# Kernel tuning notes

Measured on AMD Instinct MI355X. Metric: run time of the kernel, lower is better.

Reference implementation:

```python
import jax, jax.numpy as jnp
import numpy as np

R = 1  # local_window_radius (kernel = 2R+1 = 3)


def setup_inputs() -> dict:
    key = jax.random.key(0)
    ks = jax.random.split(key, 4)
    b, c, h, w, v = 4, 128, 96, 192, 2
    scale = 1.0 / np.sqrt(c).astype(np.float32)
    return {
        "feature0": jax.random.normal(ks[0], (b, c, h, w), jnp.float32),
        "flow": jax.random.normal(ks[1], (b, v, h, w), jnp.float32),
        "Wq": jax.random.normal(ks[2], (c, c), jnp.float32) * scale,
        "bq": jnp.zeros((c,), jnp.float32),
        "Wk": jax.random.normal(ks[3], (c, c), jnp.float32) * scale,
        "bk": jnp.zeros((c,), jnp.float32),
    }


def _windows(x, r):
    # x: [b, C, h, w] -> [b, h, w, C, k^2], zero-padded 3x3 neighborhoods.
    # Window element order matches F.unfold: row-major over (dy, dx).
    b, C, h, w = x.shape
    xp = jnp.pad(x, ((0, 0), (0, 0), (r, r), (r, r)))
    k = 2 * r + 1
    wins = [xp[:, :, dy:dy + h, dx:dx + w] for dy in range(k) for dx in range(k)]
    return jnp.stack(wins, axis=-1).transpose(0, 2, 3, 1, 4)


def reference(feature0, flow, Wq, bq, Wk, bk):
    b, c, h, w = feature0.shape
    f = feature0.transpose(0, 2, 3, 1)              # [b,h,w,c]
    q = f @ Wq.T + bq                                # q_proj -> [b,h,w,c]
    kproj = (f @ Wk.T + bk).transpose(0, 3, 1, 2)    # k_proj -> [b,c,h,w]
    k_win = _windows(kproj, R)                       # [b,h,w,c,k2]
    v_win = _windows(flow, R)                        # [b,h,w,v,k2]
    scores = jnp.einsum('bhwc,bhwck->bhwk', q, k_win) / jnp.sqrt(jnp.asarray(c, q.dtype))
    prob = jax.nn.softmax(scores, axis=-1)           # [b,h,w,k2]
    out = jnp.einsum('bhwk,bhwvk->bhwv', prob, v_win)
    return out.transpose(0, 3, 1, 2)                 # [b,v,h,w]
```

## Files before the change

kernel.cpp:

```cpp
#include <hip/hip_runtime.h>
#include <math.h>

#define B_   4
#define C_   128
#define H_   96
#define W_   192
#define HW_  (H_*W_)

#define TH 8
#define TW 16
#define HX 18
#define HPX 180
#define SHS 136

typedef __attribute__((ext_vector_type(8))) short bf16x8;
typedef __attribute__((ext_vector_type(4))) float f32x4;

__device__ __forceinline__ unsigned short f2bf(float f) {
    unsigned u = __float_as_uint(f);
    u = (u + 0x7FFFu + ((u >> 16) & 1u)) >> 16;
    return (unsigned short)u;
}
__device__ __forceinline__ float bflo(unsigned u) { return __uint_as_float(u << 16); }
__device__ __forceinline__ float bfhi(unsigned u) { return __uint_as_float(u & 0xFFFF0000u); }

__global__ __launch_bounds__(256) void prep_kernel(
    const float* __restrict__ Wq, const float* __restrict__ Wk,
    const float* __restrict__ bq, const float* __restrict__ bk,
    short* __restrict__ Apack, float* __restrict__ u2,
    float* __restrict__ v2, float* __restrict__ c0)
{
    if (blockIdx.x < 8) {
        const int rb   = blockIdx.x;
        const int t    = threadIdx.x;
        const int lane = t & 63;
        const int row  = rb * 16 + (lane & 15);
        const int colb = (t >> 6) * 32 + (lane >> 4) * 8;
        float a[8];
#pragma unroll
        for (int j = 0; j < 8; ++j) a[j] = 0.f;
        for (int c = 0; c < C_; ++c) {
            const float wk = Wk[c * C_ + row];
            const float4 w0 = *(const float4*)(Wq + c * C_ + colb);
            const float4 w1 = *(const float4*)(Wq + c * C_ + colb + 4);
            a[0] = fmaf(wk, w0.x, a[0]); a[1] = fmaf(wk, w0.y, a[1]);
            a[2] = fmaf(wk, w0.z, a[2]); a[3] = fmaf(wk, w0.w, a[3]);
            a[4] = fmaf(wk, w1.x, a[4]); a[5] = fmaf(wk, w1.y, a[5]);
            a[6] = fmaf(wk, w1.z, a[6]); a[7] = fmaf(wk, w1.w, a[7]);
        }
        bf16x8 v;
#pragma unroll
        for (int j = 0; j < 8; ++j) v[j] = (short)f2bf(a[j]);
        *(bf16x8*)(Apack + ((size_t)rb * 256 + t) * 8) = v;
    } else {
        const int t = threadIdx.x;
        if (t < 128) {
            float a = 0.f;
            for (int c = 0; c < C_; ++c) a = fmaf(Wk[c * C_ + t], bq[c], a);
            u2[t] = a;
        } else {
            const int i = t - 128;
            float a = 0.f;
            for (int c = 0; c < C_; ++c) a = fmaf(Wq[c * C_ + i], bk[c], a);
            v2[i] = a;
        }
        if (t == 0) {
            float a = 0.f;
            for (int c = 0; c < C_; ++c) a = fmaf(bq[c], bk[c], a);
            c0[0] = a;
        }
    }
}

__global__ __launch_bounds__(256, 3) void fused_kernel(
    const float* __restrict__ f, const short* __restrict__ Apack,
    const float* __restrict__ u2v, const float* __restrict__ v2v,
    const float* __restrict__ c0p, const float* __restrict__ flow,
    float* __restrict__ out)
{
    __shared__ unsigned short sH[HPX * SHS];
    __shared__ float sS[TH][TW][9];

    const int t    = threadIdx.x;
    const int lane = t & 63;
    const int w    = t >> 6;
    const int g    = lane >> 4, p = lane & 15;

    const int wg  = blockIdx.x;
    const int idx = (wg & 7) * 72 + (wg >> 3);
    const int b   = idx / 144;
    const int rem = idx - b * 144;
    const int ty  = rem / 12, tx = rem - ty * 12;
    const int y0  = ty * TH, x0 = tx * TW;
    const float* fb = f + (size_t)b * C_ * HW_;

#pragma unroll
    for (int it = 0; it < 12; ++it) {
        const int gi = it * 256 + t;
        if (gi < HPX * 16) {
            const int c8 = gi / HPX;
            const int px = gi - c8 * HPX;
            const int hy = px / HX;
            const int hx = px - hy * HX;
            const int gy = y0 + hy - 1, gx = x0 + hx - 1;
            bf16x8 v = {0, 0, 0, 0, 0, 0, 0, 0};
            if ((gy >= 0) && (gy < H_) && (gx >= 0) && (gx < W_)) {
                const float* src = fb + gy * W_ + gx;
#pragma unroll
                for (int j = 0; j < 8; ++j)
                    v[j] = (short)f2bf(src[(size_t)(c8 * 8 + j) * HW_]);
            }
            *(bf16x8*)(sH + px * SHS + c8 * 8) = v;
        }
    }
    __syncthreads();

    f32x4 acc[8][2];
#pragma unroll
    for (int rb = 0; rb < 8; ++rb)
#pragma unroll
        for (int cf = 0; cf < 2; ++cf) acc[rb][cf] = (f32x4){0.f, 0.f, 0.f, 0.f};

#pragma unroll
    for (int ks = 0; ks < 4; ++ks) {
        bf16x8 afr[8];
#pragma unroll
        for (int rb = 0; rb < 8; ++rb)
            afr[rb] = *(const bf16x8*)(Apack + ((size_t)((rb * 4 + ks) * 64 + lane)) * 8);
        bf16x8 bfr[2];
#pragma unroll
        for (int cf = 0; cf < 2; ++cf) {
            const int hpx = (2 * w + cf + 1) * HX + (p + 1);
            bfr[cf] = *(const bf16x8*)(sH + hpx * SHS + (ks * 4 + g) * 8);
        }
#pragma unroll
        for (int rb = 0; rb < 8; ++rb)
#pragma unroll
            for (int cf = 0; cf < 2; ++cf)
                acc[rb][cf] = __builtin_amdgcn_mfma_f32_16x16x32_bf16(
                    afr[rb], bfr[cf], acc[rb][cf], 0, 0, 0);
    }

    const int L0 = ((lane & 16) << 1) | p;
    const int L1 = L0 + 16;
    bf16x8 aS[2][4];
#pragma unroll
    for (int cf = 0; cf < 2; ++cf) {
        uint2 pk[8];
#pragma unroll
        for (int rb = 0; rb < 8; ++rb) {
            const f32x4 uu = *(const f32x4*)(u2v + rb * 16 + g * 4);
            const f32x4 vv = acc[rb][cf] + uu;
            pk[rb].x = (unsigned)f2bf(vv[0]) | ((unsigned)f2bf(vv[1]) << 16);
            pk[rb].y = (unsigned)f2bf(vv[2]) | ((unsigned)f2bf(vv[3]) << 16);
        }
#pragma unroll
        for (int ks = 0; ks < 4; ++ks) {
            int dw[4];
#pragma unroll
            for (int dd = 0; dd < 4; ++dd) {
                const int v0 = (dd & 1) ? (int)pk[2 * ks].y     : (int)pk[2 * ks].x;
                const int v1 = (dd & 1) ? (int)pk[2 * ks + 1].y : (int)pk[2 * ks + 1].x;
                const int sl = (dd & 2) ? L1 : L0;
                const int w0 = __shfl(v0, sl, 64);
                const int w1 = __shfl(v1, sl, 64);
                dw[dd] = (g & 2) ? w1 : w0;
            }
            int4 qv = make_int4(dw[0], dw[1], dw[2], dw[3]);
            aS[cf][ks] = *(bf16x8*)&qv;
        }
    }

#pragma unroll
    for (int cf = 0; cf < 2; ++cf) {
        const int y = 2 * w + cf;
#pragma unroll
        for (int dy = 0; dy < 3; ++dy) {
            const int hyy = y + dy;
            f32x4 s0 = (f32x4){0.f, 0.f, 0.f, 0.f};
            f32x4 s1 = (f32x4){0.f, 0.f, 0.f, 0.f};
#pragma unroll
            for (int ks = 0; ks < 4; ++ks) {
                const int hpx0 = hyy * HX + p;
                const bf16x8 b0 = *(const bf16x8*)(sH + hpx0 * SHS + (ks * 4 + g) * 8);
                const bf16x8 b1 = *(const bf16x8*)(sH + (hpx0 + 2) * SHS + (ks * 4 + g) * 8);
                s0 = __builtin_amdgcn_mfma_f32_16x16x32_bf16(aS[cf][ks], b0, s0, 0, 0, 0);
                s1 = __builtin_amdgcn_mfma_f32_16x16x32_bf16(aS[cf][ks], b1, s1, 0, 0, 0);
            }
#pragma unroll
            for (int i = 0; i < 4; ++i) {
                const int x = g * 4 + i;
                const float val = (g < 2) ? s0[i] : s1[i];
                const int   d   = (g < 2) ? (p - x) : (x - p);
                const int   n9  = (g < 2) ? (dy * 3 + d) : (dy * 3 + 2 - d);
                if ((unsigned)d <= 2u) sS[y][x][n9] = val;
            }
        }
    }

    const int r  = (lane >> 4) & 1;
    const int v  = lane >> 5;
    const int xl = lane & 15;
    const int yl = 2 * w + r;
    const int gy = y0 + yl, gx = x0 + xl;

    float beta = 0.f;
    const bool edge = (gx == 0) | (gx == W_ - 1) | (gy == 0) | (gy == H_ - 1);
    if (edge) {
        const int hpx = (yl + 1) * HX + (xl + 1);
#pragma unroll
        for (int c8 = 0; c8 < 16; ++c8) {
            const uint4 hv = *(const uint4*)(sH + hpx * SHS + c8 * 8);
            const float4 va = *(const float4*)(v2v + c8 * 8);
            const float4 vb = *(const float4*)(v2v + c8 * 8 + 4);
            beta += bflo(hv.x) * va.x + bfhi(hv.x) * va.y
                  + bflo(hv.y) * va.z + bfhi(hv.y) * va.w
                  + bflo(hv.z) * vb.x + bfhi(hv.z) * vb.y
                  + bflo(hv.w) * vb.z + bfhi(hv.w) * vb.w;
        }
        beta += *c0p;
    }

    const float scale = 0.08838834764831845f;
    float sv[9], mk[9];
    int spn[9];
    float m = -1e30f;
#pragma unroll
    for (int n = 0; n < 9; ++n) {
        const int yn = gy + n / 3 - 1, xn = gx + n % 3 - 1;
        const bool ok = (yn >= 0) && (yn < H_) && (xn >= 0) && (xn < W_);
        mk[n]  = ok ? 1.f : 0.f;
        spn[n] = ok ? yn * W_ + xn : gy * W_ + gx;
        sv[n]  = ok ? (sS[yl][xl][n] + beta) * scale : 0.f;
        m = fmaxf(m, sv[n]);
    }
    float e[9], sum = 0.f;
#pragma unroll
    for (int n = 0; n < 9; ++n) { e[n] = __expf(sv[n] - m); sum += e[n]; }
    const float inv = 1.f / sum;

    const float* f0 = flow + ((size_t)b * 2 + v) * HW_;
    float o = 0.f;
#pragma unroll
    for (int n = 0; n < 9; ++n) o += e[n] * mk[n] * f0[spn[n]];
    out[((size_t)b * 2 + v) * HW_ + gy * W_ + gx] = o * inv;
}

extern "C" void kernel_launch(void* const* d_in, const int* in_sizes, int n_in,
                              void* d_out, int out_size, void* d_ws, size_t ws_size,
                              hipStream_t stream) {
    const float* f   = (const float*)d_in[0];
    const float* flw = (const float*)d_in[1];
    const float* Wq  = (const float*)d_in[2];
    const float* bq  = (const float*)d_in[3];
    const float* Wk  = (const float*)d_in[4];
    const float* bk  = (const float*)d_in[5];
    float* out = (float*)d_out;

    short* Apack = (short*)d_ws;
    float* u2    = (float*)(Apack + 128 * 128);
    float* v2    = u2 + 128;
    float* c0    = v2 + 128;

    prep_kernel<<<9, 256, 0, stream>>>(Wq, Wk, bq, bk, Apack, u2, v2, c0);
    fused_kernel<<<576, 256, 0, stream>>>(f, Apack, u2, v2, c0, flw, out);
}
```

Measured before the change: 36.84 us.

## Use 512-thread blocks with one tile row per wave in fused kernel

Doubles the fused kernel's block size to 8 waves, with each wave handling one tile row instead of two. This halves per-wave MFMA accumulators and register pressure, and the halo load now spans all 512 threads. The prep kernel's weight-product loop is unrolled by four to batch its loads, and f32-to-bf16 conversion now uses the library intrinsic. In exchange, half the lanes in the final softmax and flow gather idle, and the larger blocks with high LDS use may limit how many blocks fit per CU.

```diff
diff --git a/kernel.cpp b/kernel.cpp
--- a/kernel.cpp
+++ b/kernel.cpp
@@ -1,4 +1,5 @@
 #include <hip/hip_runtime.h>
+#include <hip/hip_bf16.h>
 #include <math.h>
 
 #define B_   4
@@ -17,9 +18,8 @@
 typedef __attribute__((ext_vector_type(4))) float f32x4;
 
 __device__ __forceinline__ unsigned short f2bf(float f) {
-    unsigned u = __float_as_uint(f);
-    u = (u + 0x7FFFu + ((u >> 16) & 1u)) >> 16;
-    return (unsigned short)u;
+    __hip_bfloat16 h = __float2bfloat16(f);
+    return *(unsigned short*)&h;
 }
 __device__ __forceinline__ float bflo(unsigned u) { return __uint_as_float(u << 16); }
 __device__ __forceinline__ float bfhi(unsigned u) { return __uint_as_float(u & 0xFFFF0000u); }
@@ -39,14 +39,23 @@
         float a[8];
 #pragma unroll
         for (int j = 0; j < 8; ++j) a[j] = 0.f;
-        for (int c = 0; c < C_; ++c) {
-            const float wk = Wk[c * C_ + row];
-            const float4 w0 = *(const float4*)(Wq + c * C_ + colb);
-            const float4 w1 = *(const float4*)(Wq + c * C_ + colb + 4);
-            a[0] = fmaf(wk, w0.x, a[0]); a[1] = fmaf(wk, w0.y, a[1]);
-            a[2] = fmaf(wk, w0.z, a[2]); a[3] = fmaf(wk, w0.w, a[3]);
-            a[4] = fmaf(wk, w1.x, a[4]); a[5] = fmaf(wk, w1.y, a[5]);
-            a[6] = fmaf(wk, w1.z, a[6]); a[7] = fmaf(wk, w1.w, a[7]);
+#pragma unroll 2
+        for (int c = 0; c < C_; c += 4) {
+            float wk[4];
+            float4 wv[4][2];
+#pragma unroll
+            for (int u = 0; u < 4; ++u) {
+                wk[u] = Wk[(c + u) * C_ + row];
+                wv[u][0] = *(const float4*)(Wq + (c + u) * C_ + colb);
+                wv[u][1] = *(const float4*)(Wq + (c + u) * C_ + colb + 4);
+            }
+#pragma unroll
+            for (int u = 0; u < 4; ++u) {
+                a[0] = fmaf(wk[u], wv[u][0].x, a[0]); a[1] = fmaf(wk[u], wv[u][0].y, a[1]);
+                a[2] = fmaf(wk[u], wv[u][0].z, a[2]); a[3] = fmaf(wk[u], wv[u][0].w, a[3]);
+                a[4] = fmaf(wk[u], wv[u][1].x, a[4]); a[5] = fmaf(wk[u], wv[u][1].y, a[5]);
+                a[6] = fmaf(wk[u], wv[u][1].z, a[6]); a[7] = fmaf(wk[u], wv[u][1].w, a[7]);
+            }
         }
         bf16x8 v;
 #pragma unroll
@@ -72,7 +81,7 @@
     }
 }
 
-__global__ __launch_bounds__(256, 3) void fused_kernel(
+__global__ __launch_bounds__(512, 6) void fused_kernel(
     const float* __restrict__ f, const short* __restrict__ Apack,
     const float* __restrict__ u2v, const float* __restrict__ v2v,
     const float* __restrict__ c0p, const float* __restrict__ flow,
@@ -95,8 +104,8 @@
     const float* fb = f + (size_t)b * C_ * HW_;
 
 #pragma unroll
-    for (int it = 0; it < 12; ++it) {
-        const int gi = it * 256 + t;
+    for (int it = 0; it < 6; ++it) {
+        const int gi = it * 512 + t;
         if (gi < HPX * 16) {
             const int c8 = gi / HPX;
             const int px = gi - c8 * HPX;
@@ -115,99 +124,81 @@
     }
     __syncthreads();
 
-    f32x4 acc[8][2];
-#pragma unroll
-    for (int rb = 0; rb < 8; ++rb)
-#pragma unroll
-        for (int cf = 0; cf < 2; ++cf) acc[rb][cf] = (f32x4){0.f, 0.f, 0.f, 0.f};
+    f32x4 acc[8];
+#pragma unroll
+    for (int rb = 0; rb < 8; ++rb) acc[rb] = (f32x4){0.f, 0.f, 0.f, 0.f};
 
 #pragma unroll
     for (int ks = 0; ks < 4; ++ks) {
-        bf16x8 afr[8];
-#pragma unroll
-        for (int rb = 0; rb < 8; ++rb)
-            afr[rb] = *(const bf16x8*)(Apack + ((size_t)((rb * 4 + ks) * 64 + lane)) * 8);
-        bf16x8 bfr[2];
-#pragma unroll
-        for (int cf = 0; cf < 2; ++cf) {
-            const int hpx = (2 * w + cf + 1) * HX + (p + 1);
-            bfr[cf] = *(const bf16x8*)(sH + hpx * SHS + (ks * 4 + g) * 8);
-        }
-#pragma unroll
-        for (int rb = 0; rb < 8; ++rb)
-#pragma unroll
-            for (int cf = 0; cf < 2; ++cf)
-                acc[rb][cf] = __builtin_amdgcn_mfma_f32_16x16x32_bf16(
-                    afr[rb], bfr[cf], acc[rb][cf], 0, 0, 0);
+        const int hpx = (w + 1) * HX + (p + 1);
+        const bf16x8 bfr = *(const bf16x8*)(sH + hpx * SHS + (ks * 4 + g) * 8);
+#pragma unroll
+        for (int rb = 0; rb < 8; ++rb) {
+            const bf16x8 afr = *(const bf16x8*)(Apack +
+                ((size_t)((rb * 4 + ks) * 64 + lane)) * 8);
+            acc[rb] = __builtin_amdgcn_mfma_f32_16x16x32_bf16(afr, bfr, acc[rb], 0, 0, 0);
+        }
     }
 
     const int L0 = ((lane & 16) << 1) | p;
     const int L1 = L0 + 16;
-    bf16x8 aS[2][4];
-#pragma unroll
-    for (int cf = 0; cf < 2; ++cf) {
-        uint2 pk[8];
-#pragma unroll
-        for (int rb = 0; rb < 8; ++rb) {
-            const f32x4 uu = *(const f32x4*)(u2v + rb * 16 + g * 4);
-            const f32x4 vv = acc[rb][cf] + uu;
-            pk[rb].x = (unsigned)f2bf(vv[0]) | ((unsigned)f2bf(vv[1]) << 16);
-            pk[rb].y = (unsigned)f2bf(vv[2]) | ((unsigned)f2bf(vv[3]) << 16);
-        }
+    uint2 pk[8];
+#pragma unroll
+    for (int rb = 0; rb < 8; ++rb) {
+        const f32x4 uu = *(const f32x4*)(u2v + rb * 16 + g * 4);
+        const f32x4 vv = acc[rb] + uu;
+        pk[rb].x = (unsigned)f2bf(vv[0]) | ((unsigned)f2bf(vv[1]) << 16);
+        pk[rb].y = (unsigned)f2bf(vv[2]) | ((unsigned)f2bf(vv[3]) << 16);
+    }
+    bf16x8 aS[4];
+#pragma unroll
+    for (int ks = 0; ks < 4; ++ks) {
+        int dw[4];
+#pragma unroll
+        for (int dd = 0; dd < 4; ++dd) {
+            const int v0 = (dd & 1) ? (int)pk[2 * ks].y     : (int)pk[2 * ks].x;
+            const int v1 = (dd & 1) ? (int)pk[2 * ks + 1].y : (int)pk[2 * ks + 1].x;
+            const int sl = (dd & 2) ? L1 : L0;
+            const int w0 = __shfl(v0, sl, 64);
+            const int w1 = __shfl(v1, sl, 64);
+            dw[dd] = (g & 2) ? w1 : w0;
+        }
+        int4 qv = make_int4(dw[0], dw[1], dw[2], dw[3]);
+        aS[ks] = *(bf16x8*)&qv;
+    }
+
+#pragma unroll
+    for (int dy = 0; dy < 3; ++dy) {
+        const int hyy = w + dy;
+        f32x4 s0 = (f32x4){0.f, 0.f, 0.f, 0.f};
+        f32x4 s1 = (f32x4){0.f, 0.f, 0.f, 0.f};
 #pragma unroll
         for (int ks = 0; ks < 4; ++ks) {
-            int dw[4];
-#pragma unroll
-            for (int dd = 0; dd < 4; ++dd) {
-                const int v0 = (dd & 1) ? (int)pk[2 * ks].y     : (int)pk[2 * ks].x;
-                const int v1 = (dd & 1) ? (int)pk[2 * ks + 1].y : (int)pk[2 * ks + 1].x;
-                const int sl = (dd & 2) ? L1 : L0;
-                const int w0 = __shfl(v0, sl, 64);
-                const int w1 = __shfl(v1, sl, 64);
-                dw[dd] = (g & 2) ? w1 : w0;
-            }
-            int4 qv = make_int4(dw[0], dw[1], dw[2], dw[3]);
-            aS[cf][ks] = *(bf16x8*)&qv;
-        }
-    }
-
-#pragma unroll
-    for (int cf = 0; cf < 2; ++cf) {
-        const int y = 2 * w + cf;
-#pragma unroll
-        for (int dy = 0; dy < 3; ++dy) {
-            const int hyy = y + dy;
-            f32x4 s0 = (f32x4){0.f, 0.f, 0.f, 0.f};
-            f32x4 s1 = (f32x4){0.f, 0.f, 0.f, 0.f};
-#pragma unroll
-            for (int ks = 0; ks < 4; ++ks) {
-                const int hpx0 = hyy * HX + p;
-                const bf16x8 b0 = *(const bf16x8*)(sH + hpx0 * SHS + (ks * 4 + g) * 8);
-                const bf16x8 b1 = *(const bf16x8*)(sH + (hpx0 + 2) * SHS + (ks * 4 + g) * 8);
-                s0 = __builtin_amdgcn_mfma_f32_16x16x32_bf16(aS[cf][ks], b0, s0, 0, 0, 0);
-                s1 = __builtin_amdgcn_mfma_f32_16x16x32_bf16(aS[cf][ks], b1, s1, 0, 0, 0);
-            }
-#pragma unroll
-            for (int i = 0; i < 4; ++i) {
-                const int x = g * 4 + i;
-                const float val = (g < 2) ? s0[i] : s1[i];
-                const int   d   = (g < 2) ? (p - x) : (x - p);
-                const int   n9  = (g < 2) ? (dy * 3 + d) : (dy * 3 + 2 - d);
-                if ((unsigned)d <= 2u) sS[y][x][n9] = val;
-            }
+            const int hpx0 = hyy * HX + p;
+            const bf16x8 b0 = *(const bf16x8*)(sH + hpx0 * SHS + (ks * 4 + g) * 8);
+            const bf16x8 b1 = *(const bf16x8*)(sH + (hpx0 + 2) * SHS + (ks * 4 + g) * 8);
+            s0 = __builtin_amdgcn_mfma_f32_16x16x32_bf16(aS[ks], b0, s0, 0, 0, 0);
+            s1 = __builtin_amdgcn_mfma_f32_16x16x32_bf16(aS[ks], b1, s1, 0, 0, 0);
+        }
+#pragma unroll
+        for (int i = 0; i < 4; ++i) {
+            const int x = g * 4 + i;
+            const float val = (g < 2) ? s0[i] : s1[i];
+            const int   d   = (g < 2) ? (p - x) : (x - p);
+            const int   n9  = (g < 2) ? (dy * 3 + d) : (dy * 3 + 2 - d);
+            if ((unsigned)d <= 2u) sS[w][x][n9] = val;
         }
     }
 
     const int r  = (lane >> 4) & 1;
     const int v  = lane >> 5;
     const int xl = lane & 15;
-    const int yl = 2 * w + r;
-    const int gy = y0 + yl, gx = x0 + xl;
+    const int gy = y0 + w, gx = x0 + xl;
 
     float beta = 0.f;
     const bool edge = (gx == 0) | (gx == W_ - 1) | (gy == 0) | (gy == H_ - 1);
     if (edge) {
-        const int hpx = (yl + 1) * HX + (xl + 1);
+        const int hpx = (w + 1) * HX + (xl + 1);
 #pragma unroll
         for (int c8 = 0; c8 < 16; ++c8) {
             const uint4 hv = *(const uint4*)(sH + hpx * SHS + c8 * 8);
@@ -231,7 +222,7 @@
         const bool ok = (yn >= 0) && (yn < H_) && (xn >= 0) && (xn < W_);
         mk[n]  = ok ? 1.f : 0.f;
         spn[n] = ok ? yn * W_ + xn : gy * W_ + gx;
-        sv[n]  = ok ? (sS[yl][xl][n] + beta) * scale : 0.f;
+        sv[n]  = ok ? (sS[w][xl][n] + beta) * scale : 0.f;
         m = fmaxf(m, sv[n]);
     }
     float e[9], sum = 0.f;
@@ -239,11 +230,13 @@
     for (int n = 0; n < 9; ++n) { e[n] = __expf(sv[n] - m); sum += e[n]; }
     const float inv = 1.f / sum;
 
-    const float* f0 = flow + ((size_t)b * 2 + v) * HW_;
-    float o = 0.f;
-#pragma unroll
-    for (int n = 0; n < 9; ++n) o += e[n] * mk[n] * f0[spn[n]];
-    out[((size_t)b * 2 + v) * HW_ + gy * W_ + gx] = o * inv;
+    if (r == 0) {
+        const float* f0 = flow + ((size_t)b * 2 + v) * HW_;
+        float o = 0.f;
+#pragma unroll
+        for (int n = 0; n < 9; ++n) o += e[n] * mk[n] * f0[spn[n]];
+        out[((size_t)b * 2 + v) * HW_ + gy * W_ + gx] = o * inv;
+    }
 }
 
 extern "C" void kernel_launch(void* const* d_in, const int* in_sizes, int n_in,
@@ -263,5 +256,5 @@
     float* c0    = v2 + 128;
 
     prep_kernel<<<9, 256, 0, stream>>>(Wq, Wk, bq, bk, Apack, u2, v2, c0);
-    fused_kernel<<<576, 256, 0, stream>>>(f, Apack, u2, v2, c0, flw, out);
-}
+    fused_kernel<<<576, 512, 0, stream>>>(f, Apack, u2, v2, c0, flw, out);
+}
```

Measured after the change: 38.83 us. 5.4% more time.
